# Kernel tuning notes

Measured on AMD Instinct MI355X. Metric: run time of the kernel, lower is better.

## Reference

```python
import jax, jax.numpy as jnp
import numpy as np

NUM_HEADS = 16
HEAD_DIM = 128
SEQ_LEN = 2048
MAX_SEQ_LEN = 2048
NUM_PATTERNS = 4
BATCH = 4


def setup_inputs() -> dict:
    key = jax.random.key(0)
    ks = jax.random.split(key, 8)
    Q = jax.random.normal(ks[0], (BATCH, NUM_HEADS, SEQ_LEN, HEAD_DIM), dtype=jnp.float32)
    K = jax.random.normal(ks[1], (BATCH, NUM_HEADS, SEQ_LEN, HEAD_DIM), dtype=jnp.float32)
    V = jax.random.normal(ks[2], (BATCH, NUM_HEADS, SEQ_LEN, HEAD_DIM), dtype=jnp.float32)
    # SparseAttentionLearner params
    pattern_masks = jax.random.normal(ks[3], (NUM_PATTERNS, MAX_SEQ_LEN, MAX_SEQ_LEN), dtype=jnp.float32) * 0.1
    # pattern_selector: Linear(3,32) -> ReLU -> Linear(32,num_patterns)
    sel_w1 = jax.random.normal(ks[4], (3, 32), dtype=jnp.float32) * (1.0 / np.sqrt(3.0))
    sel_b1 = jax.random.normal(ks[5], (32,), dtype=jnp.float32) * 0.1
    sel_w2 = jax.random.normal(ks[6], (32, NUM_PATTERNS), dtype=jnp.float32) * (1.0 / np.sqrt(32.0))
    sel_b2 = jax.random.normal(ks[7], (NUM_PATTERNS,), dtype=jnp.float32) * 0.1
    return {"Q": Q, "K": K, "V": V, "pattern_masks": pattern_masks,
            "sel_w1": sel_w1, "sel_b1": sel_b1, "sel_w2": sel_w2, "sel_b2": sel_b2}


def reference(Q, K, V, pattern_masks, sel_w1, sel_b1, sel_w2, sel_b2):
    B, H, S, D = Q.shape
    # Per-head pattern-selector features: [seq_len/max_seq_len, head_id/12, 0.5]
    head_ids = jnp.arange(H, dtype=jnp.float32)
    feats = jnp.stack([
        jnp.full((H,), S / float(MAX_SEQ_LEN), dtype=jnp.float32),
        head_ids / 12.0,
        jnp.full((H,), 0.5, dtype=jnp.float32),
    ], axis=-1)  # [H, 3]
    hidden = jax.nn.relu(feats @ sel_w1 + sel_b1)          # [H, 32]
    logits = hidden @ sel_w2 + sel_b2                       # [H, num_patterns]
    pat_idx = jnp.argmax(logits, axis=-1)                   # [H]
    # Learned binary sparse masks per head: sigmoid > 0.5
    sel_masks = jnp.take(pattern_masks, pat_idx, axis=0)[:, :S, :S]  # [H, S, S]
    binary_mask = (jax.nn.sigmoid(sel_masks) > 0.5).astype(Q.dtype)   # [H, S, S]
    # Sparse attention: scores multiplied (not masked_fill) by binary mask
    scores = jnp.einsum('bhsd,bhtd->bhst', Q, K) / jnp.sqrt(jnp.float32(D)).astype(Q.dtype)
    scores = scores * binary_mask[None]
    attn = jax.nn.softmax(scores, axis=-1)
    out = jnp.einsum('bhst,bhtd->bhsd', attn, V)
    return out
```

## Files before the change

kernel.cpp:

```cpp
#include <hip/hip_runtime.h>
#include <hip/hip_bf16.h>
#include <math.h>

#define BATCH 4
#define NHEADS 16
#define SEQ 2048
#define HDIM 128
#define NPAT 4

#define BM 128
#define BN 64
#define NTHREADS 256
#define NKT (SEQ / BN)
#define TILE_BYTES 16384
#define NBLOCKS (BATCH * NHEADS * (SEQ / BM))

typedef _Float16 f16x8 __attribute__((ext_vector_type(8)));
typedef _Float16 f16x4 __attribute__((ext_vector_type(4)));
typedef float floatx4 __attribute__((ext_vector_type(4)));

typedef const __attribute__((address_space(1))) void gvoid_t;
typedef __attribute__((address_space(3))) void lvoid_t;

__global__ void sel_kernel(const float* __restrict__ w1, const float* __restrict__ b1,
                           const float* __restrict__ w2, const float* __restrict__ b2,
                           int* __restrict__ pat_idx, int* __restrict__ used) {
  int h = threadIdx.x;
  if (h < NPAT) used[h] = 0;
  __syncthreads();
  if (h >= NHEADS) return;
  float f0 = 1.0f;
  float f1 = (float)h / 12.0f;
  float f2 = 0.5f;
  float acc[NPAT] = {b2[0], b2[1], b2[2], b2[3]};
  for (int j = 0; j < 32; ++j) {
    float hj = f0 * w1[j] + f1 * w1[32 + j] + f2 * w1[64 + j] + b1[j];
    hj = fmaxf(hj, 0.0f);
    for (int p = 0; p < NPAT; ++p) acc[p] += hj * w2[j * NPAT + p];
  }
  int best = 0;
  float bv = acc[0];
  for (int p = 1; p < NPAT; ++p) {
    if (acc[p] > bv) { bv = acc[p]; best = p; }
  }
  pat_idx[h] = best;
  atomicOr(&used[best], 1);
}

__device__ __forceinline__ bool sig_gt_half(float x) {
  float t = (float)exp(-(double)x);
  float s = 1.0f / (1.0f + t);
  return s > 0.5f;
}

__global__ void bin_kernel(const float* __restrict__ pm, unsigned int* __restrict__ bits,
                           const int* __restrict__ used) {
  int pat = blockIdx.x >> 9;
  if (!used[pat]) return;
  int t = blockIdx.x * blockDim.x + threadIdx.x;
  const float4* s4 = (const float4*)(pm + (size_t)t * 32);
  unsigned int w = 0;
#pragma unroll
  for (int i = 0; i < 8; ++i) {
    float4 v = s4[i];
    float e[4] = {v.x, v.y, v.z, v.w};
#pragma unroll
    for (int j = 0; j < 4; ++j) {
      bool b;
      if (fabsf(e[j]) < 1e-5f) b = sig_gt_half(e[j]);
      else                     b = (e[j] > 0.0f);
      w |= (b ? 1u : 0u) << (i * 4 + j);
    }
  }
  bits[t] = w;
}

__global__ __launch_bounds__(256) void prep_k(const float* __restrict__ K,
                                              _Float16* __restrict__ Kp) {
  size_t q0 = ((size_t)blockIdx.x * 256 + threadIdx.x) * 16;
  int tile = (int)(q0 >> 14);
  int p = (int)(q0 & 16383);
  int r = p >> 8;
  int cb = (p & 255) ^ ((r & 7) << 4);
  const float* src = K + ((size_t)tile * 64 + r) * HDIM + (cb >> 1);
  float4 a = ((const float4*)src)[0];
  float4 b = ((const float4*)src)[1];
  f16x8 f;
  f[0] = (_Float16)a.x; f[1] = (_Float16)a.y; f[2] = (_Float16)a.z; f[3] = (_Float16)a.w;
  f[4] = (_Float16)b.x; f[5] = (_Float16)b.y; f[6] = (_Float16)b.z; f[7] = (_Float16)b.w;
  *(f16x8*)((char*)Kp + q0) = f;
}

__global__ __launch_bounds__(256) void prep_vt(const float* __restrict__ V,
                                               _Float16* __restrict__ Vt) {
  __shared__ _Float16 tile[64][140];
  const int t = threadIdx.x;
  const float* vsrc = V + (size_t)blockIdx.x * 64 * HDIM;
#pragma unroll
  for (int i = 0; i < 8; ++i) {
    int idx = i * 256 + t;
    int kc = idx >> 5, c4 = idx & 31;
    float4 v = ((const float4*)(vsrc + kc * HDIM))[c4];
    f16x4 f;
    f[0] = (_Float16)v.x; f[1] = (_Float16)v.y; f[2] = (_Float16)v.z; f[3] = (_Float16)v.w;
    *(f16x4*)&tile[kc][c4 * 4] = f;
  }
  __syncthreads();
  char* dst = (char*)Vt + (size_t)blockIdx.x * TILE_BYTES;
#pragma unroll
  for (int i = 0; i < 4; ++i) {
    int p = (i * 256 + t) * 16;
    int d = p >> 7;
    int cp = (p & 127) >> 4;
    int clog = cp ^ (d & 7);
    int q = clog & 3, ks = clog >> 2;
    int T16 = ((q >> 1) * 2 + ks) << 4;
    f16x8 f;
#pragma unroll
    for (int j = 0; j < 8; ++j) {
      int qsel = (j < 4) ? q : (q ^ 2);
      int kc = T16 + qsel * 4 + (j & 3);
      f[j] = tile[kc][d];
    }
    *(f16x8*)(dst + p) = f;
  }
}

__global__ __launch_bounds__(NTHREADS, 3) void flash_kernel(
    const float* __restrict__ Q, const _Float16* __restrict__ Kp,
    const _Float16* __restrict__ Vt, const unsigned int* __restrict__ bits,
    const int* __restrict__ pat_idx, float* __restrict__ out) {
  __shared__ alignas(16) char kv_raw[2 * TILE_BYTES];
  __shared__ unsigned int maskw[BM][2];

  const int tid = threadIdx.x;
  const int wave = tid >> 6;
  const int lane = tid & 63;
  const int l16 = lane & 15;
  const int quad = lane >> 4;
  const int swz = l16 & 7;

  int bid = (int)blockIdx.x;
  bid = (bid & 7) * (NBLOCKS / 8) + (bid >> 3);
  const int bh = bid >> 4;
  const int qt = bid & 15;
  const int h = bh & (NHEADS - 1);
  const int qbase = qt * BM;
  const int pat = pat_idx[h];

  const float SCL = 0.08838834764831845f * 1.4426950408889634f;
  const float P_MIN = 6.103515625e-05f;

  f16x8 qf[2][4];
#pragma unroll
  for (int mt = 0; mt < 2; ++mt) {
    const int row = qbase + wave * 32 + mt * 16 + l16;
    const float* qp = Q + ((size_t)bh * SEQ + row) * HDIM;
#pragma unroll
    for (int ks = 0; ks < 4; ++ks) {
      const float4* p4 = (const float4*)(qp + ks * 32 + quad * 8);
      float4 a = p4[0], c = p4[1];
      f16x8 f;
      f[0] = (_Float16)a.x; f[1] = (_Float16)a.y; f[2] = (_Float16)a.z; f[3] = (_Float16)a.w;
      f[4] = (_Float16)c.x; f[5] = (_Float16)c.y; f[6] = (_Float16)c.z; f[7] = (_Float16)c.w;
      qf[mt][ks] = f;
    }
  }

  floatx4 o_acc[2][8];
#pragma unroll
  for (int mt = 0; mt < 2; ++mt)
#pragma unroll
    for (int n = 0; n < 8; ++n) o_acc[mt][n] = (floatx4){0.f, 0.f, 0.f, 0.f};
  float m_run[2] = {-INFINITY, -INFINITY};
  float l_run[2] = {0.0f, 0.0f};

  const char* kg = (const char*)Kp + (size_t)bh * NKT * TILE_BYTES;
  const char* vg = (const char*)Vt + (size_t)bh * NKT * TILE_BYTES;
  const unsigned int* bits_p = bits + ((size_t)pat * SEQ + qbase) * (SEQ / 32);

  for (int kt = 0; kt < NKT; ++kt) {
    __syncthreads();
    {
      const char* kgt = kg + (size_t)kt * TILE_BYTES + wave * 1024 + lane * 16;
      const char* vgt = vg + (size_t)kt * TILE_BYTES + wave * 1024 + lane * 16;
      char* kl = kv_raw + wave * 1024;
      char* vl = kv_raw + TILE_BYTES + wave * 1024;
#pragma unroll
      for (int i = 0; i < 4; ++i) {
        __builtin_amdgcn_global_load_lds((gvoid_t*)(kgt + i * 4096),
                                         (lvoid_t*)(kl + i * 4096), 16, 0, 0);
        __builtin_amdgcn_global_load_lds((gvoid_t*)(vgt + i * 4096),
                                         (lvoid_t*)(vl + i * 4096), 16, 0, 0);
      }
      int mr = tid >> 1, mw = tid & 1;
      maskw[mr][mw] = bits_p[(size_t)mr * (SEQ / 32) + kt * 2 + mw];
    }
    __syncthreads();

    floatx4 sf[4][2];
#pragma unroll
    for (int t = 0; t < 4; ++t)
#pragma unroll
      for (int mt = 0; mt < 2; ++mt) sf[t][mt] = (floatx4){0.f, 0.f, 0.f, 0.f};
    __builtin_amdgcn_s_setprio(1);
#pragma unroll
    for (int t = 0; t < 4; ++t) {
      const char* krow = kv_raw + ((t * 16 + l16) << 8);
#pragma unroll
      for (int ks = 0; ks < 4; ++ks) {
        f16x8 kf = *(const f16x8*)(krow + ((((ks << 2) | quad) ^ swz) << 4));
#pragma unroll
        for (int mt = 0; mt < 2; ++mt)
          sf[t][mt] = __builtin_amdgcn_mfma_f32_16x16x32_f16(kf, qf[mt][ks], sf[t][mt], 0, 0, 0);
      }
    }
    __builtin_amdgcn_s_setprio(0);

    f16x4 hq[4][2];
    float alpha[2];
#pragma unroll
    for (int mt = 0; mt < 2; ++mt) {
      const int rl = wave * 32 + mt * 16 + l16;
      const unsigned w0 = maskw[rl][0], w1 = maskw[rl][1];
#pragma unroll
      for (int t = 0; t < 4; ++t) {
        const unsigned wd = (t & 2) ? w1 : w0;
        const int base = ((t & 1) << 4) + (quad << 2);
#pragma unroll
        for (int r = 0; r < 4; ++r) {
          float s = sf[t][mt][r];
          sf[t][mt][r] = ((wd >> (base + r)) & 1u) ? s * SCL : 0.0f;
        }
      }
      float mx = sf[0][mt][0];
#pragma unroll
      for (int t = 0; t < 4; ++t)
#pragma unroll
        for (int r = 0; r < 4; ++r) mx = fmaxf(mx, sf[t][mt][r]);
      mx = fmaxf(mx, __shfl_xor(mx, 16));
      mx = fmaxf(mx, __shfl_xor(mx, 32));
      const float m_old = m_run[mt];
      const float m_new = fmaxf(m_old, mx);
      const float a = exp2f(m_old - m_new);
      alpha[mt] = a;
      m_run[mt] = m_new;
      float ps = 0.0f;
#pragma unroll
      for (int t = 0; t < 4; ++t) {
#pragma unroll
        for (int r = 0; r < 4; ++r) {
          float p = exp2f(sf[t][mt][r] - m_new);
          if (p < P_MIN) p = 0.0f;
          _Float16 hh = (_Float16)p;
          hq[t][mt][r] = hh;
          ps += (float)hh;
        }
      }
      ps += __shfl_xor(ps, 16);
      ps += __shfl_xor(ps, 32);
      l_run[mt] = l_run[mt] * a + ps;
    }

#pragma unroll
    for (int mt = 0; mt < 2; ++mt) {
#pragma unroll
      for (int r = 0; r < 4; ++r) {
        const float ac = __shfl(alpha[mt], (quad << 2) | r, 16);
#pragma unroll
        for (int n = 0; n < 8; ++n) o_acc[mt][n][r] *= ac;
      }
    }

    __builtin_amdgcn_s_setprio(1);
#pragma unroll
    for (int ks = 0; ks < 2; ++ks) {
      f16x8 pa[2];
#pragma unroll
      for (int mt = 0; mt < 2; ++mt) {
        f16x4 hk = (quad & 2) ? hq[ks + 2][mt] : hq[ks][mt];
        f16x4 hs = (quad & 2) ? hq[ks][mt] : hq[ks + 2][mt];
        union { f16x4 v; unsigned u[2]; } K_, S_;
        K_.v = hk; S_.v = hs;
        unsigned p0 = (unsigned)__shfl_xor((int)S_.u[0], 32);
        unsigned p1 = (unsigned)__shfl_xor((int)S_.u[1], 32);
        union { unsigned u[4]; f16x8 v; } P_;
        P_.u[0] = K_.u[0]; P_.u[1] = K_.u[1]; P_.u[2] = p0; P_.u[3] = p1;
        pa[mt] = P_.v;
      }
#pragma unroll
      for (int nt = 0; nt < 8; ++nt) {
        const char* vrow = kv_raw + TILE_BYTES + ((nt * 16 + l16) << 7);
        f16x8 vb = *(const f16x8*)(vrow + ((((ks << 2) | quad) ^ swz) << 4));
#pragma unroll
        for (int mt = 0; mt < 2; ++mt)
          o_acc[mt][nt] = __builtin_amdgcn_mfma_f32_16x16x32_f16(pa[mt], vb, o_acc[mt][nt], 0, 0, 0);
      }
    }
    __builtin_amdgcn_s_setprio(0);
  }

#pragma unroll
  for (int mt = 0; mt < 2; ++mt) {
#pragma unroll
    for (int r = 0; r < 4; ++r) {
      const float lv = __shfl(l_run[mt], (quad << 2) | r, 16);
      const float inv = 1.0f / lv;
      const int row = qbase + wave * 32 + mt * 16 + quad * 4 + r;
      float* og = out + ((size_t)bh * SEQ + row) * HDIM + l16;
#pragma unroll
      for (int n = 0; n < 8; ++n) og[n * 16] = o_acc[mt][n][r] * inv;
    }
  }
}

extern "C" void kernel_launch(void* const* d_in, const int* in_sizes, int n_in,
                              void* d_out, int out_size, void* d_ws, size_t ws_size,
                              hipStream_t stream) {
  const float* Q  = (const float*)d_in[0];
  const float* K  = (const float*)d_in[1];
  const float* V  = (const float*)d_in[2];
  const float* pm = (const float*)d_in[3];
  const float* w1 = (const float*)d_in[4];
  const float* b1 = (const float*)d_in[5];
  const float* w2 = (const float*)d_in[6];
  const float* b2 = (const float*)d_in[7];
  float* out = (float*)d_out;

  int* pat_idx = (int*)d_ws;
  int* used = (int*)((char*)d_ws + 256);
  unsigned int* bits = (unsigned int*)((char*)d_ws + 4096);
  _Float16* Kp = (_Float16*)((char*)d_ws + 4096 + 2097152);
  _Float16* Vt = (_Float16*)((char*)d_ws + 4096 + 2097152 + 33554432);

  sel_kernel<<<1, 64, 0, stream>>>(w1, b1, w2, b2, pat_idx, used);
  bin_kernel<<<(NPAT * SEQ * (SEQ / 32)) / 256, 256, 0, stream>>>(pm, bits, used);
  prep_k<<<(BATCH * NHEADS * NKT * 1024) / 256, 256, 0, stream>>>(K, Kp);
  prep_vt<<<BATCH * NHEADS * NKT, 256, 0, stream>>>(V, Vt);
  flash_kernel<<<NBLOCKS, NTHREADS, 0, stream>>>(Q, Kp, Vt, bits, pat_idx, out);
}
```

Baseline: 525.7 us.

## Double-buffer K/V and mask tiles, skip unchanged-max rescale, use native exp2

The flash kernel now double-buffers the K/V tiles and mask words in LDS. The next tile is prefetched with global_load_lds, including the mask words, while the current tile is computed, leaving one barrier per iteration. The output and row-sum rescale is skipped when no row max increases, and exp2 uses the hardware builtin. The bin kernel takes a fast sign-test path and falls back to the slow double-precision sigmoid only in rare near-zero cases. The cost is doubled LDS use and a launch-bounds drop from 3 to 2 blocks per SM.

```diff
diff --git a/kernel.cpp b/kernel.cpp
--- a/kernel.cpp
+++ b/kernel.cpp
@@ -21,6 +21,12 @@
 
 typedef const __attribute__((address_space(1))) void gvoid_t;
 typedef __attribute__((address_space(3))) void lvoid_t;
+
+#if __has_builtin(__builtin_amdgcn_exp2f)
+#define EXP2(x) __builtin_amdgcn_exp2f(x)
+#else
+#define EXP2(x) exp2f(x)
+#endif
 
 __global__ void sel_kernel(const float* __restrict__ w1, const float* __restrict__ b1,
                            const float* __restrict__ w2, const float* __restrict__ b2,
@@ -47,7 +53,7 @@
   atomicOr(&used[best], 1);
 }
 
-__device__ __forceinline__ bool sig_gt_half(float x) {
+__device__ __attribute__((noinline)) bool sig_gt_half_slow(float x) {
   float t = (float)exp(-(double)x);
   float s = 1.0f / (1.0f + t);
   return s > 0.5f;
@@ -60,16 +66,29 @@
   int t = blockIdx.x * blockDim.x + threadIdx.x;
   const float4* s4 = (const float4*)(pm + (size_t)t * 32);
   unsigned int w = 0;
+  bool anyneed = false;
 #pragma unroll
   for (int i = 0; i < 8; ++i) {
     float4 v = s4[i];
     float e[4] = {v.x, v.y, v.z, v.w};
 #pragma unroll
     for (int j = 0; j < 4; ++j) {
-      bool b;
-      if (fabsf(e[j]) < 1e-5f) b = sig_gt_half(e[j]);
-      else                     b = (e[j] > 0.0f);
-      w |= (b ? 1u : 0u) << (i * 4 + j);
+      anyneed |= (fabsf(e[j]) < 1e-5f);
+      w |= ((e[j] > 0.0f) ? 1u : 0u) << (i * 4 + j);
+    }
+  }
+  if (__ballot(anyneed)) {
+    if (anyneed) {
+      w = 0;
+#pragma unroll 1
+      for (int i = 0; i < 8; ++i) {
+        float4 v = s4[i];
+        float e[4] = {v.x, v.y, v.z, v.w};
+        for (int j = 0; j < 4; ++j) {
+          bool b = (fabsf(e[j]) < 1e-5f) ? sig_gt_half_slow(e[j]) : (e[j] > 0.0f);
+          w |= (b ? 1u : 0u) << (i * 4 + j);
+        }
+      }
     }
   }
   bits[t] = w;
@@ -126,12 +145,12 @@
   }
 }
 
-__global__ __launch_bounds__(NTHREADS, 3) void flash_kernel(
+__global__ __launch_bounds__(NTHREADS, 2) void flash_kernel(
     const float* __restrict__ Q, const _Float16* __restrict__ Kp,
     const _Float16* __restrict__ Vt, const unsigned int* __restrict__ bits,
     const int* __restrict__ pat_idx, float* __restrict__ out) {
-  __shared__ alignas(16) char kv_raw[2 * TILE_BYTES];
-  __shared__ unsigned int maskw[BM][2];
+  __shared__ alignas(16) char kv_raw[2][2 * TILE_BYTES];
+  __shared__ unsigned int maskw[2][BM][2];
 
   const int tid = threadIdx.x;
   const int wave = tid >> 6;
@@ -151,6 +170,29 @@
   const float SCL = 0.08838834764831845f * 1.4426950408889634f;
   const float P_MIN = 6.103515625e-05f;
 
+  const unsigned int* bits_p = bits + ((size_t)pat * SEQ + qbase) * (SEQ / 32);
+  const char* kgbase = (const char*)Kp + (size_t)bh * NKT * TILE_BYTES + wave * 1024 + lane * 16;
+  const char* vgbase = (const char*)Vt + (size_t)bh * NKT * TILE_BYTES + wave * 1024 + lane * 16;
+  const unsigned int* mgbase = bits_p + (size_t)(wave * 32 + (lane >> 1)) * (SEQ / 32) + (lane & 1);
+
+  auto stage = [&](int nb, int kt) {
+    const char* kgt = kgbase + (size_t)kt * TILE_BYTES;
+    const char* vgt = vgbase + (size_t)kt * TILE_BYTES;
+    char* kl = &kv_raw[nb][0] + wave * 1024;
+    char* vl = &kv_raw[nb][TILE_BYTES] + wave * 1024;
+#pragma unroll
+    for (int i = 0; i < 4; ++i) {
+      __builtin_amdgcn_global_load_lds((gvoid_t*)(kgt + i * 4096),
+                                       (lvoid_t*)(kl + i * 4096), 16, 0, 0);
+      __builtin_amdgcn_global_load_lds((gvoid_t*)(vgt + i * 4096),
+                                       (lvoid_t*)(vl + i * 4096), 16, 0, 0);
+    }
+    __builtin_amdgcn_global_load_lds((gvoid_t*)(mgbase + 2 * kt),
+                                     (lvoid_t*)&maskw[nb][wave * 32][0], 4, 0, 0);
+  };
+
+  stage(0, 0);
+
   f16x8 qf[2][4];
 #pragma unroll
   for (int mt = 0; mt < 2; ++mt) {
@@ -175,28 +217,14 @@
   float m_run[2] = {-INFINITY, -INFINITY};
   float l_run[2] = {0.0f, 0.0f};
 
-  const char* kg = (const char*)Kp + (size_t)bh * NKT * TILE_BYTES;
-  const char* vg = (const char*)Vt + (size_t)bh * NKT * TILE_BYTES;
-  const unsigned int* bits_p = bits + ((size_t)pat * SEQ + qbase) * (SEQ / 32);
+  __syncthreads();
+  int cur = 0;
 
   for (int kt = 0; kt < NKT; ++kt) {
-    __syncthreads();
-    {
-      const char* kgt = kg + (size_t)kt * TILE_BYTES + wave * 1024 + lane * 16;
-      const char* vgt = vg + (size_t)kt * TILE_BYTES + wave * 1024 + lane * 16;
-      char* kl = kv_raw + wave * 1024;
-      char* vl = kv_raw + TILE_BYTES + wave * 1024;
-#pragma unroll
-      for (int i = 0; i < 4; ++i) {
-        __builtin_amdgcn_global_load_lds((gvoid_t*)(kgt + i * 4096),
-                                         (lvoid_t*)(kl + i * 4096), 16, 0, 0);
-        __builtin_amdgcn_global_load_lds((gvoid_t*)(vgt + i * 4096),
-                                         (lvoid_t*)(vl + i * 4096), 16, 0, 0);
-      }
-      int mr = tid >> 1, mw = tid & 1;
-      maskw[mr][mw] = bits_p[(size_t)mr * (SEQ / 32) + kt * 2 + mw];
-    }
-    __syncthreads();
+    if (kt + 1 < NKT) stage(cur ^ 1, kt + 1);
+
+    const char* kbuf = &kv_raw[cur][0];
+    const char* vbuf = &kv_raw[cur][TILE_BYTES];
 
     floatx4 sf[4][2];
 #pragma unroll
@@ -206,7 +234,7 @@
     __builtin_amdgcn_s_setprio(1);
 #pragma unroll
     for (int t = 0; t < 4; ++t) {
-      const char* krow = kv_raw + ((t * 16 + l16) << 8);
+      const char* krow = kbuf + ((t * 16 + l16) << 8);
 #pragma unroll
       for (int ks = 0; ks < 4; ++ks) {
         f16x8 kf = *(const f16x8*)(krow + ((((ks << 2) | quad) ^ swz) << 4));
@@ -217,12 +245,10 @@
     }
     __builtin_amdgcn_s_setprio(0);
 
-    f16x4 hq[4][2];
-    float alpha[2];
 #pragma unroll
     for (int mt = 0; mt < 2; ++mt) {
       const int rl = wave * 32 + mt * 16 + l16;
-      const unsigned w0 = maskw[rl][0], w1 = maskw[rl][1];
+      const unsigned w0 = maskw[cur][rl][0], w1 = maskw[cur][rl][1];
 #pragma unroll
       for (int t = 0; t < 4; ++t) {
         const unsigned wd = (t & 2) ? w1 : w0;
@@ -233,24 +259,49 @@
           sf[t][mt][r] = ((wd >> (base + r)) & 1u) ? s * SCL : 0.0f;
         }
       }
-      float mx = sf[0][mt][0];
-#pragma unroll
-      for (int t = 0; t < 4; ++t)
-#pragma unroll
-        for (int r = 0; r < 4; ++r) mx = fmaxf(mx, sf[t][mt][r]);
-      mx = fmaxf(mx, __shfl_xor(mx, 16));
-      mx = fmaxf(mx, __shfl_xor(mx, 32));
-      const float m_old = m_run[mt];
-      const float m_new = fmaxf(m_old, mx);
-      const float a = exp2f(m_old - m_new);
-      alpha[mt] = a;
-      m_run[mt] = m_new;
+    }
+    float mx0 = sf[0][0][0], mx1 = sf[0][1][0];
+#pragma unroll
+    for (int t = 0; t < 4; ++t)
+#pragma unroll
+      for (int r = 0; r < 4; ++r) {
+        mx0 = fmaxf(mx0, sf[t][0][r]);
+        mx1 = fmaxf(mx1, sf[t][1][r]);
+      }
+    mx0 = fmaxf(mx0, __shfl_xor(mx0, 16));
+    mx0 = fmaxf(mx0, __shfl_xor(mx0, 32));
+    mx1 = fmaxf(mx1, __shfl_xor(mx1, 16));
+    mx1 = fmaxf(mx1, __shfl_xor(mx1, 32));
+
+    if (!__all((mx0 <= m_run[0]) && (mx1 <= m_run[1]))) {
+      float alpha[2];
+      const float mn0 = fmaxf(m_run[0], mx0);
+      const float mn1 = fmaxf(m_run[1], mx1);
+      alpha[0] = EXP2(m_run[0] - mn0);
+      alpha[1] = EXP2(m_run[1] - mn1);
+      m_run[0] = mn0; m_run[1] = mn1;
+      l_run[0] *= alpha[0]; l_run[1] *= alpha[1];
+#pragma unroll
+      for (int mt = 0; mt < 2; ++mt) {
+#pragma unroll
+        for (int r = 0; r < 4; ++r) {
+          const float ac = __shfl(alpha[mt], (quad << 2) | r, 16);
+#pragma unroll
+          for (int n = 0; n < 8; ++n) o_acc[mt][n][r] *= ac;
+        }
+      }
+    }
+
+    f16x4 hq[4][2];
+#pragma unroll
+    for (int mt = 0; mt < 2; ++mt) {
+      const float mrow = m_run[mt];
       float ps = 0.0f;
 #pragma unroll
       for (int t = 0; t < 4; ++t) {
 #pragma unroll
         for (int r = 0; r < 4; ++r) {
-          float p = exp2f(sf[t][mt][r] - m_new);
+          float p = EXP2(sf[t][mt][r] - mrow);
           if (p < P_MIN) p = 0.0f;
           _Float16 hh = (_Float16)p;
           hq[t][mt][r] = hh;
@@ -259,17 +310,7 @@
       }
       ps += __shfl_xor(ps, 16);
       ps += __shfl_xor(ps, 32);
-      l_run[mt] = l_run[mt] * a + ps;
-    }
-
-#pragma unroll
-    for (int mt = 0; mt < 2; ++mt) {
-#pragma unroll
-      for (int r = 0; r < 4; ++r) {
-        const float ac = __shfl(alpha[mt], (quad << 2) | r, 16);
-#pragma unroll
-        for (int n = 0; n < 8; ++n) o_acc[mt][n][r] *= ac;
-      }
+      l_run[mt] += ps;
     }
 
     __builtin_amdgcn_s_setprio(1);
@@ -290,7 +331,7 @@
       }
 #pragma unroll
       for (int nt = 0; nt < 8; ++nt) {
-        const char* vrow = kv_raw + TILE_BYTES + ((nt * 16 + l16) << 7);
+        const char* vrow = vbuf + ((nt * 16 + l16) << 7);
         f16x8 vb = *(const f16x8*)(vrow + ((((ks << 2) | quad) ^ swz) << 4));
 #pragma unroll
         for (int mt = 0; mt < 2; ++mt)
@@ -298,6 +339,9 @@
       }
     }
     __builtin_amdgcn_s_setprio(0);
+
+    __syncthreads();
+    cur ^= 1;
   }
 
 #pragma unroll
```

New measurement: 479.3 us. 8.8% less time.
